# Optimization experiments

Hardware: AMD Instinct MI355X
Metric: run time of the kernel (lower is better)

## Reference

```python
import jax, jax.numpy as jnp
import numpy as np

D = 256
H = 4
HD = D // H


def setup_inputs() -> dict:
    key = jax.random.key(0)
    ks = jax.random.split(key, 12)
    A, T = 64, 512
    s = 1.0 / np.sqrt(D)
    return {
        "features": jax.random.normal(ks[0], (A, T, D), jnp.float32),
        "positions": jax.random.normal(ks[1], (A, T, 2), jnp.float32),
        "Wq": jax.random.normal(ks[2], (D, D), jnp.float32) * s,
        "bq": jnp.zeros((D,), jnp.float32),
        "Wk": jax.random.normal(ks[3], (D, D), jnp.float32) * s,
        "bk": jnp.zeros((D,), jnp.float32),
        "Wv": jax.random.normal(ks[4], (D, D), jnp.float32) * s,
        "bv": jnp.zeros((D,), jnp.float32),
        "Wo": jax.random.normal(ks[5], (D, D), jnp.float32) * s,
        "bo": jnp.zeros((D,), jnp.float32),
        "max_distance": 2,
        "time_window": 64,
    }


def _sparse_mask(positions, max_distance, time_window):
    # positions: [A, T, 2] -> allowed [A, T, T]
    A, T, _ = positions.shape
    diff = positions[:, :, None, :] - positions[:, None, :, :]  # [A,T,T,2]
    dist2 = jnp.sum(diff * diff, axis=-1)                       # [A,T,T]
    t = jnp.arange(T)
    tmask = jnp.abs(t[:, None] - t[None, :]) <= time_window      # [T,T]
    return (dist2 <= float(max_distance) ** 2) & tmask[None]     # [A,T,T]


def reference(features, positions, Wq, bq, Wk, bk, Wv, bv, Wo, bo,
              max_distance, time_window):
    A, T, Dm = features.shape
    allowed = _sparse_mask(positions, max_distance, time_window)  # [A,T,T]
    q = features @ Wq.T + bq
    k = features @ Wk.T + bk
    v = features @ Wv.T + bv
    # split heads: [A, T, H, HD]
    q = q.reshape(A, T, H, HD)
    k = k.reshape(A, T, H, HD)
    v = v.reshape(A, T, H, HD)
    scale = 1.0 / np.sqrt(HD)
    scores = jnp.einsum("athd,ashd->ahts", q, k) * scale          # [A,H,T,T]
    scores = jnp.where(allowed[:, None], scores, -jnp.inf)
    attn = jax.nn.softmax(scores, axis=-1)
    out = jnp.einsum("ahts,ashd->athd", attn, v).reshape(A, T, Dm)
    return out @ Wo.T + bo
```

## Files before the change

### kernel.cpp

```cpp
#include <hip/hip_runtime.h>
#include <hip/hip_bf16.h>
#include <cstdint>
#include <cstddef>

typedef __attribute__((ext_vector_type(8))) _Float16 half8;
typedef __attribute__((ext_vector_type(4))) _Float16 half4v;
typedef __attribute__((ext_vector_type(4))) float floatx4;

#define MFMA16(a, b, c) __builtin_amdgcn_mfma_f32_16x16x32_f16((a), (b), (c), 0, 0, 0)

#define NFEAT 8388608
#define NW    65536

__global__ __launch_bounds__(256) void convert_kernel(
    const float* __restrict__ feat, const float* __restrict__ wq,
    const float* __restrict__ wk, const float* __restrict__ wv,
    const float* __restrict__ wo, _Float16* __restrict__ out)
{
    long tid  = (long)blockIdx.x * blockDim.x + threadIdx.x;
    long base = tid * 4;
    if (base >= (long)NFEAT + 4L * NW) return;
    const float* src;
    long off;
    if (base < NFEAT) { src = feat; off = base; }
    else {
        long r = base - NFEAT;
        int  w = (int)(r >> 16);
        off = r & (NW - 1);
        src = (w == 0) ? wq : (w == 1) ? wk : (w == 2) ? wv : wo;
    }
    float4 v = *(const float4*)(src + off);
    half4v h = { (_Float16)v.x, (_Float16)v.y, (_Float16)v.z, (_Float16)v.w };
    *(half4v*)(out + base) = h;
}

template <bool OUT_HALF>
__device__ __forceinline__ void gemm_core2(
    const _Float16* __restrict__ X, const _Float16* __restrict__ W,
    const float* __restrict__ bias, void* __restrict__ Cptr, int bm)
{
    __shared__ _Float16 Xs[128 * 40];
    __shared__ _Float16 Ws[256 * 40];

    const int tid  = threadIdx.x;
    const int lane = tid & 63, wid = tid >> 6;
    const int quad = lane >> 4, l16 = lane & 15;
    const int wm = wid & 1, wn = wid >> 1;

    floatx4 acc[4][8] = {};
    const _Float16* Xg = X + (size_t)bm * 128 * 256;

    for (int k0 = 0; k0 < 256; k0 += 32) {
#pragma unroll
        for (int i = 0; i < 2; ++i) {
            int c = tid + 256 * i;
            int row = c >> 2, col = (c & 3) * 8;
            *(half8*)(&Xs[row * 40 + col]) =
                *(const half8*)(Xg + (size_t)row * 256 + k0 + col);
        }
#pragma unroll
        for (int i = 0; i < 4; ++i) {
            int c = tid + 256 * i;
            int row = c >> 2, col = (c & 3) * 8;
            *(half8*)(&Ws[row * 40 + col]) =
                *(const half8*)(W + (size_t)row * 256 + k0 + col);
        }
        __syncthreads();

        half8 af[4], bf[8];
#pragma unroll
        for (int mi = 0; mi < 4; ++mi)
            af[mi] = *(const half8*)(&Xs[(wm * 64 + mi * 16 + l16) * 40 + quad * 8]);
#pragma unroll
        for (int ni = 0; ni < 8; ++ni)
            bf[ni] = *(const half8*)(&Ws[(wn * 128 + ni * 16 + l16) * 40 + quad * 8]);
#pragma unroll
        for (int mi = 0; mi < 4; ++mi)
#pragma unroll
            for (int ni = 0; ni < 8; ++ni)
                acc[mi][ni] = MFMA16(af[mi], bf[ni], acc[mi][ni]);
        __syncthreads();
    }

#pragma unroll
    for (int ni = 0; ni < 8; ++ni) {
        int col = wn * 128 + ni * 16 + l16;
        float bv = bias[col];
#pragma unroll
        for (int mi = 0; mi < 4; ++mi) {
#pragma unroll
            for (int r = 0; r < 4; ++r) {
                int row = bm * 128 + wm * 64 + mi * 16 + quad * 4 + r;
                float v = acc[mi][ni][r] + bv;
                if (OUT_HALF)
                    ((_Float16*)Cptr)[(size_t)row * 256 + col] = (_Float16)v;
                else
                    ((float*)Cptr)[(size_t)row * 256 + col] = v;
            }
        }
    }
}

__global__ __launch_bounds__(256, 2) void qkv_gemm(
    const _Float16* __restrict__ featH, const _Float16* __restrict__ WH,
    const float* __restrict__ bq, const float* __restrict__ bk,
    const float* __restrict__ bv,
    _Float16* __restrict__ Qb, _Float16* __restrict__ Kb, _Float16* __restrict__ Vb)
{
    int z = blockIdx.x;
    const _Float16* W = WH + (size_t)z * NW;
    const float* bias = (z == 0) ? bq : (z == 1) ? bk : bv;
    _Float16* out    = (z == 0) ? Qb : (z == 1) ? Kb : Vb;
    gemm_core2<true>(featH, W, bias, out, blockIdx.y);
}

__global__ __launch_bounds__(256, 2) void out_gemm(
    const _Float16* __restrict__ attnH, const _Float16* __restrict__ WoH,
    const float* __restrict__ bo, float* __restrict__ out)
{
    gemm_core2<false>(attnH, WoH, bo, out, blockIdx.y);
}

__global__ __launch_bounds__(256) void attn_kernel(
    const _Float16* __restrict__ Qb, const _Float16* __restrict__ Kb,
    const _Float16* __restrict__ Vb, const float* __restrict__ positions,
    const int* __restrict__ mdp, const int* __restrict__ twp,
    _Float16* __restrict__ attnb)
{
    const int qt = blockIdx.x, h = blockIdx.y, a = blockIdx.z;
    const int q0 = qt * 64;
    const int s_base = q0 - 64;
    const int tid = threadIdx.x, lane = tid & 63, wid = tid >> 6;
    const int quad = lane >> 4, l16 = lane & 15;

    __shared__ _Float16 KPs[192 * 72];
    __shared__ _Float16 Vt[64 * 200];

    const size_t abase = (size_t)a * 512;

#pragma unroll
    for (int i = 0; i < 6; ++i) {
        int c  = tid + 256 * i;
        int si = c >> 3, col = (c & 7) * 8;
        int sc = min(max(s_base + si, 0), 511);
        *(half8*)(&KPs[si * 72 + col]) =
            *(const half8*)(Kb + (abase + sc) * 256 + h * 64 + col);
    }
#pragma unroll
    for (int i = 0; i < 6; ++i) {
        int c  = tid + 256 * i;
        int si = c % 192;
        int d0 = (c / 192) * 8;
        int sc = min(max(s_base + si, 0), 511);
        half8 v = *(const half8*)(Vb + (abase + sc) * 256 + h * 64 + d0);
#pragma unroll
        for (int j = 0; j < 8; ++j) Vt[(d0 + j) * 200 + si] = v[j];
    }
    __syncthreads();

    const int md = *mdp, tw = *twp;
    const float md2 = (float)(md * md);

    const size_t qrow = abase + q0 + wid * 16 + l16;
    half8 aq0 = *(const half8*)(Qb + qrow * 256 + h * 64 + quad * 8);
    half8 aq1 = *(const half8*)(Qb + qrow * 256 + h * 64 + 32 + quad * 8);

    float qpx[4], qpy[4];
    int trow[4];
#pragma unroll
    for (int r = 0; r < 4; ++r) {
        int m = wid * 16 + quad * 4 + r;
        trow[r] = q0 + m;
        float2 qp = *(const float2*)(positions + (abase + q0 + m) * 2);
        qpx[r] = qp.x;
        qpy[r] = qp.y;
    }

    floatx4 S[12];
#pragma unroll
    for (int j = 0; j < 12; ++j) {
        half8 bk0 = *(const half8*)(&KPs[(j * 16 + l16) * 72 + quad * 8]);
        half8 bk1 = *(const half8*)(&KPs[(j * 16 + l16) * 72 + 32 + quad * 8]);
        floatx4 acc = {};
        acc = MFMA16(aq0, bk0, acc);
        acc = MFMA16(aq1, bk1, acc);
        int si = j * 16 + l16;
        int sr = s_base + si;
        int sc = min(max(sr, 0), 511);
        float2 kp = *(const float2*)(positions + (abase + sc) * 2);
        bool svalid = (sr >= 0) && (sr < 512);
#pragma unroll
        for (int r = 0; r < 4; ++r) {
            float dx = qpx[r] - kp.x, dy = qpy[r] - kp.y;
            float d2 = dx * dx + dy * dy;
            int dt = trow[r] - sr; dt = dt < 0 ? -dt : dt;
            bool ok = svalid && (d2 <= md2) && (dt <= tw);
            S[j][r] = ok ? acc[r] * 0.125f : -1e30f;
        }
    }

    float minv[4];
#pragma unroll
    for (int r = 0; r < 4; ++r) {
        float m = -1e30f;
#pragma unroll
        for (int j = 0; j < 12; ++j) m = fmaxf(m, S[j][r]);
        m = fmaxf(m, __shfl_xor(m, 1));
        m = fmaxf(m, __shfl_xor(m, 2));
        m = fmaxf(m, __shfl_xor(m, 4));
        m = fmaxf(m, __shfl_xor(m, 8));
        float l = 0.f;
#pragma unroll
        for (int j = 0; j < 12; ++j) {
            float p = __expf(S[j][r] - m);
            S[j][r] = p;
            l += p;
        }
        l += __shfl_xor(l, 1);
        l += __shfl_xor(l, 2);
        l += __shfl_xor(l, 4);
        l += __shfl_xor(l, 8);
        minv[r] = 1.0f / l;
    }

    __syncthreads();

    _Float16* Ps = KPs + wid * 16 * 200;
#pragma unroll
    for (int j = 0; j < 12; ++j)
#pragma unroll
        for (int r = 0; r < 4; ++r)
            Ps[(quad * 4 + r) * 200 + j * 16 + l16] = (_Float16)(S[j][r] * minv[r]);

    half8 af[6];
#pragma unroll
    for (int k = 0; k < 6; ++k)
        af[k] = *(const half8*)(&Ps[l16 * 200 + k * 32 + quad * 8]);
#pragma unroll
    for (int n = 0; n < 4; ++n) {
        floatx4 accO = {};
#pragma unroll
        for (int k = 0; k < 6; ++k) {
            half8 bv = *(const half8*)(&Vt[(n * 16 + l16) * 200 + k * 32 + quad * 8]);
            accO = MFMA16(af[k], bv, accO);
        }
#pragma unroll
        for (int r = 0; r < 4; ++r) {
            int row = q0 + wid * 16 + quad * 4 + r;
            attnb[(abase + row) * 256 + h * 64 + n * 16 + l16] = (_Float16)accO[r];
        }
    }
}

extern "C" void kernel_launch(void* const* d_in, const int* in_sizes, int n_in,
                              void* d_out, int out_size, void* d_ws, size_t ws_size,
                              hipStream_t stream)
{
    const float* feat = (const float*)d_in[0];
    const float* pos  = (const float*)d_in[1];
    const float* Wq   = (const float*)d_in[2];
    const float* bq   = (const float*)d_in[3];
    const float* Wk   = (const float*)d_in[4];
    const float* bk   = (const float*)d_in[5];
    const float* Wv   = (const float*)d_in[6];
    const float* bv   = (const float*)d_in[7];
    const float* Wo   = (const float*)d_in[8];
    const float* bo   = (const float*)d_in[9];
    const int*   md   = (const int*)d_in[10];
    const int*   tw   = (const int*)d_in[11];
    float*       out  = (float*)d_out;

    _Float16* ws    = (_Float16*)d_ws;
    _Float16* featH = ws;
    _Float16* WH    = featH + NFEAT;
    _Float16* Qb    = WH + 4 * NW;
    _Float16* Kb    = Qb + NFEAT;
    _Float16* Vb    = Kb + NFEAT;
    _Float16* attnH = featH;

    convert_kernel<<<8448, 256, 0, stream>>>(feat, Wq, Wk, Wv, Wo, ws);

    dim3 gqkv(3, 256);
    qkv_gemm<<<gqkv, 256, 0, stream>>>(featH, WH, bq, bk, bv, Qb, Kb, Vb);

    dim3 gattn(8, 4, 64);
    attn_kernel<<<gattn, 256, 0, stream>>>(Qb, Kb, Vb, pos, md, tw, attnH);

    dim3 gout(1, 256);
    out_gemm<<<gout, 256, 0, stream>>>(attnH, WH + 3 * (size_t)NW, bo, out);
}
```

Before: 187.5 us.

## Use direct global-to-LDS loads with XOR swizzle and 128x128 GEMM tiles

```diff
diff --git a/kernel.cpp b/kernel.cpp
--- a/kernel.cpp
+++ b/kernel.cpp
@@ -8,6 +8,11 @@
 typedef __attribute__((ext_vector_type(4))) float floatx4;
 
 #define MFMA16(a, b, c) __builtin_amdgcn_mfma_f32_16x16x32_f16((a), (b), (c), 0, 0, 0)
+
+#define GLOAD_LDS16(g, l)                                                     \
+    __builtin_amdgcn_global_load_lds(                                         \
+        (const __attribute__((address_space(1))) void*)(g),                   \
+        (__attribute__((address_space(3))) void*)(l), 16, 0, 0)
 
 #define NFEAT 8388608
 #define NW    65536
@@ -34,57 +39,68 @@
     *(half4v*)(out + base) = h;
 }
 
+
+__device__ __forceinline__ void stage128x64(
+    const _Float16* __restrict__ src, _Float16* __restrict__ lds,
+    int wid, int lane)
+{
+#pragma unroll
+    for (int i = 0; i < 4; ++i) {
+        int grp = wid * 4 + i;
+        int row = grp * 8 + (lane >> 3);
+        int sc  = (lane & 7) ^ (row & 7);
+        GLOAD_LDS16(src + (size_t)row * 256 + sc * 8, lds + grp * 512);
+    }
+}
+
 template <bool OUT_HALF>
-__device__ __forceinline__ void gemm_core2(
+__device__ __forceinline__ void gemm128x128(
     const _Float16* __restrict__ X, const _Float16* __restrict__ W,
-    const float* __restrict__ bias, void* __restrict__ Cptr, int bm)
-{
-    __shared__ _Float16 Xs[128 * 40];
-    __shared__ _Float16 Ws[256 * 40];
+    const float* __restrict__ bias, void* __restrict__ Cptr, int bm, int bn)
+{
+    __shared__ _Float16 As[128 * 64];
+    __shared__ _Float16 Bs[128 * 64];
 
     const int tid  = threadIdx.x;
     const int lane = tid & 63, wid = tid >> 6;
     const int quad = lane >> 4, l16 = lane & 15;
     const int wm = wid & 1, wn = wid >> 1;
 
-    floatx4 acc[4][8] = {};
+    floatx4 acc[4][4] = {};
     const _Float16* Xg = X + (size_t)bm * 128 * 256;
-
-    for (int k0 = 0; k0 < 256; k0 += 32) {
-#pragma unroll
-        for (int i = 0; i < 2; ++i) {
-            int c = tid + 256 * i;
-            int row = c >> 2, col = (c & 3) * 8;
-            *(half8*)(&Xs[row * 40 + col]) =
-                *(const half8*)(Xg + (size_t)row * 256 + k0 + col);
-        }
-#pragma unroll
-        for (int i = 0; i < 4; ++i) {
-            int c = tid + 256 * i;
-            int row = c >> 2, col = (c & 3) * 8;
-            *(half8*)(&Ws[row * 40 + col]) =
-                *(const half8*)(W + (size_t)row * 256 + k0 + col);
-        }
+    const _Float16* Wg = W + (size_t)bn * 128 * 256;
+
+    for (int k0 = 0; k0 < 256; k0 += 64) {
+        stage128x64(Xg + k0, As, wid, lane);
+        stage128x64(Wg + k0, Bs, wid, lane);
         __syncthreads();
-
-        half8 af[4], bf[8];
-#pragma unroll
-        for (int mi = 0; mi < 4; ++mi)
-            af[mi] = *(const half8*)(&Xs[(wm * 64 + mi * 16 + l16) * 40 + quad * 8]);
-#pragma unroll
-        for (int ni = 0; ni < 8; ++ni)
-            bf[ni] = *(const half8*)(&Ws[(wn * 128 + ni * 16 + l16) * 40 + quad * 8]);
-#pragma unroll
-        for (int mi = 0; mi < 4; ++mi)
-#pragma unroll
-            for (int ni = 0; ni < 8; ++ni)
-                acc[mi][ni] = MFMA16(af[mi], bf[ni], acc[mi][ni]);
+#pragma unroll
+        for (int kh = 0; kh < 2; ++kh) {
+            half8 af[4], bf[4];
+#pragma unroll
+            for (int mi = 0; mi < 4; ++mi) {
+                int row = wm * 64 + mi * 16 + l16;
+                int ch  = (kh * 4 + quad) ^ (l16 & 7);
+                af[mi] = *(const half8*)(&As[row * 64 + ch * 8]);
+            }
+#pragma unroll
+            for (int ni = 0; ni < 4; ++ni) {
+                int row = wn * 64 + ni * 16 + l16;
+                int ch  = (kh * 4 + quad) ^ (l16 & 7);
+                bf[ni] = *(const half8*)(&Bs[row * 64 + ch * 8]);
+            }
+#pragma unroll
+            for (int mi = 0; mi < 4; ++mi)
+#pragma unroll
+                for (int ni = 0; ni < 4; ++ni)
+                    acc[mi][ni] = MFMA16(af[mi], bf[ni], acc[mi][ni]);
+        }
         __syncthreads();
     }
 
 #pragma unroll
-    for (int ni = 0; ni < 8; ++ni) {
-        int col = wn * 128 + ni * 16 + l16;
+    for (int ni = 0; ni < 4; ++ni) {
+        int col = bn * 128 + wn * 64 + ni * 16 + l16;
         float bv = bias[col];
 #pragma unroll
         for (int mi = 0; mi < 4; ++mi) {
@@ -101,24 +117,24 @@
     }
 }
 
-__global__ __launch_bounds__(256, 2) void qkv_gemm(
+__global__ __launch_bounds__(256) void qkv_gemm(
     const _Float16* __restrict__ featH, const _Float16* __restrict__ WH,
     const float* __restrict__ bq, const float* __restrict__ bk,
     const float* __restrict__ bv,
     _Float16* __restrict__ Qb, _Float16* __restrict__ Kb, _Float16* __restrict__ Vb)
 {
-    int z = blockIdx.x;
+    int z = blockIdx.x >> 1, bn = blockIdx.x & 1;
     const _Float16* W = WH + (size_t)z * NW;
     const float* bias = (z == 0) ? bq : (z == 1) ? bk : bv;
     _Float16* out    = (z == 0) ? Qb : (z == 1) ? Kb : Vb;
-    gemm_core2<true>(featH, W, bias, out, blockIdx.y);
-}
-
-__global__ __launch_bounds__(256, 2) void out_gemm(
+    gemm128x128<true>(featH, W, bias, out, blockIdx.y, bn);
+}
+
+__global__ __launch_bounds__(256) void out_gemm(
     const _Float16* __restrict__ attnH, const _Float16* __restrict__ WoH,
     const float* __restrict__ bo, float* __restrict__ out)
 {
-    gemm_core2<false>(attnH, WoH, bo, out, blockIdx.y);
+    gemm128x128<false>(attnH, WoH, bo, out, blockIdx.y, blockIdx.x);
 }
 
 __global__ __launch_bounds__(256) void attn_kernel(
@@ -137,6 +153,20 @@
     __shared__ _Float16 Vt[64 * 200];
 
     const size_t abase = (size_t)a * 512;
+
+    const size_t qrow = abase + q0 + wid * 16 + l16;
+    half8 aq0 = *(const half8*)(Qb + qrow * 256 + h * 64 + quad * 8);
+    half8 aq1 = *(const half8*)(Qb + qrow * 256 + h * 64 + 32 + quad * 8);
+    float qpx[4], qpy[4];
+    int trow[4];
+#pragma unroll
+    for (int r = 0; r < 4; ++r) {
+        int m = wid * 16 + quad * 4 + r;
+        trow[r] = q0 + m;
+        float2 qp = *(const float2*)(positions + (abase + q0 + m) * 2);
+        qpx[r] = qp.x;
+        qpy[r] = qp.y;
+    }
 
 #pragma unroll
     for (int i = 0; i < 6; ++i) {
@@ -160,21 +190,6 @@
 
     const int md = *mdp, tw = *twp;
     const float md2 = (float)(md * md);
-
-    const size_t qrow = abase + q0 + wid * 16 + l16;
-    half8 aq0 = *(const half8*)(Qb + qrow * 256 + h * 64 + quad * 8);
-    half8 aq1 = *(const half8*)(Qb + qrow * 256 + h * 64 + 32 + quad * 8);
-
-    float qpx[4], qpy[4];
-    int trow[4];
-#pragma unroll
-    for (int r = 0; r < 4; ++r) {
-        int m = wid * 16 + quad * 4 + r;
-        trow[r] = q0 + m;
-        float2 qp = *(const float2*)(positions + (abase + q0 + m) * 2);
-        qpx[r] = qp.x;
-        qpy[r] = qp.y;
-    }
 
     floatx4 S[12];
 #pragma unroll
@@ -280,12 +295,12 @@
 
     convert_kernel<<<8448, 256, 0, stream>>>(feat, Wq, Wk, Wv, Wo, ws);
 
-    dim3 gqkv(3, 256);
+    dim3 gqkv(6, 256);
     qkv_gemm<<<gqkv, 256, 0, stream>>>(featH, WH, bq, bk, bv, Qb, Kb, Vb);
 
     dim3 gattn(8, 4, 64);
     attn_kernel<<<gattn, 256, 0, stream>>>(Qb, Kb, Vb, pos, md, tw, attnH);
 
-    dim3 gout(1, 256);
+    dim3 gout(2, 256);
     out_gemm<<<gout, 256, 0, stream>>>(attnH, WH + 3 * (size_t)NW, bo, out);
 }
```

After: 183.6 us. -2.0%, faster.
